# Kernel tuning notes

Hardware: AMD Instinct MI355X
Metric: run time of the kernel (lower is better)

Reference implementation:

```python
import jax, jax.numpy as jnp
import numpy as np

S, T, B = 50, 50, 64
SRC_V, TRG_V = 36616, 23262
E, EH, DH = 300, 512, 1024


def setup_inputs() -> dict:
    key = jax.random.key(0)
    ks = jax.random.split(key, 20)
    n = lambda k, shape: jax.random.normal(k, shape, jnp.float32) * 0.05
    return {
        "train_src_batch": jax.random.randint(ks[0], (S, B), 0, SRC_V),
        "train_trg_batch": jax.random.randint(ks[1], (T, B), 0, TRG_V),
        "emb_en": n(ks[2], (SRC_V, E)),
        "emb_de": n(ks[3], (TRG_V, E)),
        "enc_W_ih_f": n(ks[4], (4 * EH, E)),
        "enc_W_hh_f": n(ks[5], (4 * EH, EH)),
        "enc_b_f": n(ks[6], (4 * EH,)),
        "enc_W_ih_b": n(ks[7], (4 * EH, E)),
        "enc_W_hh_b": n(ks[8], (4 * EH, EH)),
        "enc_b_b": n(ks[9], (4 * EH,)),
        "dec_W_ih": n(ks[10], (4 * DH, E + DH)),
        "dec_W_hh": n(ks[11], (4 * DH, DH)),
        "dec_b": n(ks[12], (4 * DH,)),
        "W_gen": n(ks[13], (TRG_V, DH)),
        "b_gen": n(ks[14], (TRG_V,)),
        "W_i": n(ks[15], (DH, DH)),
        "W_o": n(ks[16], (DH, 2 * DH)),
    }


def _lstm_step(x, h, c, W_ih, W_hh, b):
    # PyTorch gate order: i, f, g, o
    gates = x @ W_ih.T + h @ W_hh.T + b
    i, f, g, o = jnp.split(gates, 4, axis=-1)
    c_new = jax.nn.sigmoid(f) * c + jax.nn.sigmoid(i) * jnp.tanh(g)
    h_new = jax.nn.sigmoid(o) * jnp.tanh(c_new)
    return h_new, c_new


def _run_lstm(x_seq, W_ih, W_hh, b, hidden):
    h0 = jnp.zeros((x_seq.shape[1], hidden), x_seq.dtype)
    def step(carry, x):
        h, c = carry
        h, c = _lstm_step(x, h, c, W_ih, W_hh, b)
        return (h, c), h
    (h, c), hs = jax.lax.scan(step, (h0, h0), x_seq)
    return hs, h, c


def _forward(train_src_batch, train_trg_batch, emb_en, emb_de,
             enc_W_ih_f, enc_W_hh_f, enc_b_f, enc_W_ih_b, enc_W_hh_b, enc_b_b,
             dec_W_ih, dec_W_hh, dec_b, W_gen, b_gen, W_i, W_o):
    x = emb_en[train_src_batch]                       # [S,B,E]
    hs_f, hf, cf = _run_lstm(x, enc_W_ih_f, enc_W_hh_f, enc_b_f, EH)
    hs_b, hb, cb = _run_lstm(x[::-1], enc_W_ih_b, enc_W_hh_b, enc_b_b, EH)
    output_hs = jnp.concatenate([hs_f, hs_b[::-1]], axis=-1)  # [S,B,1024]
    # Faithful to h.contiguous().view(B,1024) on direction-major [2,B,512]
    h = jnp.reshape(jnp.stack([hf, hb], axis=0), (B, DH))
    c = jnp.reshape(jnp.stack([cf, cb], axis=0), (B, DH))

    emb_trg = emb_de[train_trg_batch[: T - 1]]        # [T-1,B,E]

    def step(carry, e):
        h, c = carry
        # score[j,b] = output_hs[j,b] . (W_i h[b])  (the diag of the original mm)
        scores = jnp.einsum('sbd,bd->sb', output_hs, h @ W_i.T)
        # legacy nn.Softmax() on 2D input -> softmax over dim=1 (batch axis)
        a = jax.nn.softmax(scores, axis=1)
        s_t = jnp.einsum('sb,sbd->bd', a, output_hs)
        c_t = jnp.tanh(jnp.concatenate([s_t, h], axis=1) @ W_o.T)
        dec_in = jnp.concatenate([c_t, e], axis=1)    # [B, 1024+300]
        h, c = _lstm_step(dec_in, h, c, dec_W_ih, dec_W_hh, dec_b)
        logp = jax.nn.log_softmax(h @ W_gen.T + b_gen, axis=1)
        return (h, c), logp

    _, outs = jax.lax.scan(step, (h, c), emb_trg)     # [T-1,B,V]
    out0 = jnp.zeros((1, B, TRG_V), outs.dtype)       # output[0] filled with 0
    return jnp.concatenate([out0, outs], axis=0)      # [T,B,V]


def reference(train_src_batch, train_trg_batch, emb_en, emb_de,
              enc_W_ih_f, enc_W_hh_f, enc_b_f, enc_W_ih_b, enc_W_hh_b, enc_b_b,
              dec_W_ih, dec_W_hh, dec_b, W_gen, b_gen, W_i, W_o):
    return _forward(train_src_batch, train_trg_batch, emb_en, emb_de,
                    enc_W_ih_f, enc_W_hh_f, enc_b_f, enc_W_ih_b, enc_W_hh_b, enc_b_b,
                    dec_W_ih, dec_W_hh, dec_b, W_gen, b_gen, W_i, W_o)
```

## Files before the change

kernel.cpp:

```cpp
#include <hip/hip_runtime.h>
#include <hip/hip_bf16.h>

#define SS 50
#define TT 50
#define BB 64
#define TRGV 23262
#define EE 300
#define EH 512
#define DH 1024

#define GMRE 3136
#define GMP 3200
#define GK 1024
#define GNRE TRGV
#define GNP 23296

typedef short bf16x8 __attribute__((ext_vector_type(8)));
typedef float f32x4 __attribute__((ext_vector_type(4)));

__device__ __forceinline__ void glds16(const void* g, void* l) {
  __builtin_amdgcn_global_load_lds(
      (const __attribute__((address_space(1))) void*)g,
      (__attribute__((address_space(3))) void*)l, 16, 0, 0);
}

__device__ __forceinline__ float sigm(float x) { return 1.f / (1.f + expf(-x)); }
__device__ __forceinline__ float sum4(f32x4 v) { return v[0] + v[1] + v[2] + v[3]; }

__device__ __forceinline__ void split2(float x, __hip_bfloat16& hi, __hip_bfloat16& lo) {
  hi = __float2bfloat16(x);
  lo = __float2bfloat16(x - __bfloat162float(hi));
}

__device__ __forceinline__ void gbar(unsigned* arrive, unsigned* gen, int nblk) {
  __syncthreads();
  unsigned g = __hip_atomic_load(gen, __ATOMIC_RELAXED, __HIP_MEMORY_SCOPE_AGENT);
  if (threadIdx.x == 0)
    __hip_atomic_store(arrive + blockIdx.x, g + 1u, __ATOMIC_RELEASE, __HIP_MEMORY_SCOPE_AGENT);
  if (blockIdx.x == 0) {
    int i = threadIdx.x;
    if (i < nblk) {
      while (__hip_atomic_load(arrive + i, __ATOMIC_RELAXED, __HIP_MEMORY_SCOPE_AGENT) < g + 1u)
        __builtin_amdgcn_s_sleep(1);
      (void)__hip_atomic_load(arrive + i, __ATOMIC_ACQUIRE, __HIP_MEMORY_SCOPE_AGENT);
    }
    __syncthreads();
    if (threadIdx.x == 0)
      __hip_atomic_store(gen, g + 1u, __ATOMIC_RELEASE, __HIP_MEMORY_SCOPE_AGENT);
  }
  if (threadIdx.x == 0) {
    while (__hip_atomic_load(gen, __ATOMIC_RELAXED, __HIP_MEMORY_SCOPE_AGENT) < g + 1u)
      __builtin_amdgcn_s_sleep(1);
    (void)__hip_atomic_load(gen, __ATOMIC_ACQUIRE, __HIP_MEMORY_SCOPE_AGENT);
  }
  __syncthreads();
}

__global__ void k_zero(float* __restrict__ p, long n) {
  long i = (long)blockIdx.x * 256 + threadIdx.x;
  if (i < n) p[i] = 0.f;
}
__global__ void k_zero_bf(__hip_bfloat16* __restrict__ p, long n) {
  long i = (long)blockIdx.x * 256 + threadIdx.x;
  if (i < n) p[i] = __float2bfloat16(0.f);
}

__global__ void k_embed(const int* __restrict__ src, const float* __restrict__ emb,
                        float* __restrict__ x) {
  int id = blockIdx.x * 256 + threadIdx.x;
  if (id >= SS * BB * EE) return;
  int sb = id / EE, e = id % EE;
  x[id] = emb[(long)src[sb] * EE + e];
}

__global__ void k_dbperm(const float* __restrict__ db, float* __restrict__ dbp) {
  int id = blockIdx.x * 256 + threadIdx.x;
  if (id >= 4096) return;
  int u = id >> 2, g = id & 3;
  dbp[id] = db[g * 1024 + u];
}

__global__ void k_split_pad(const float* __restrict__ in, int ld_in, int col_off,
                            int Kreal, int Kpad, int rows_real, long rows_pad,
                            int mode, __hip_bfloat16* __restrict__ out) {
  long id = (long)blockIdx.x * 256 + threadIdx.x;
  if (id >= rows_pad * Kpad) return;
  long r = id / Kpad;
  int k = id % Kpad;
  float v = 0.f;
  if (r < rows_real && k < Kreal) {
    if (mode == 3) {
      v = in[(long)k * ld_in + col_off + r];
    } else {
      long sr = r;
      if (mode == 1) sr = ((49 - (r >> 6)) << 6) + (r & 63);
      else if (mode == 2) sr = (long)(r & 3) * 1024 + (r >> 2);
      v = in[sr * ld_in + col_off + k];
    }
  }
  __hip_bfloat16 hi, lo;
  split2(v, hi, lo);
  out[r * 2 * Kpad + k] = hi;
  out[r * 2 * Kpad + Kpad + k] = lo;
}

__global__ void k_embgather_split(const int* __restrict__ trg, const float* __restrict__ emb,
                                  __hip_bfloat16* __restrict__ out) {
  long id = (long)blockIdx.x * 256 + threadIdx.x;
  if (id >= 3200L * 320) return;
  long r = id / 320;
  int k = id % 320;
  int t = r >> 6, b = r & 63;
  float v = 0.f;
  if (t < TT - 1 && k < EE) v = emb[(long)trg[t * BB + b] * EE + k];
  __hip_bfloat16 hi, lo;
  split2(v, hi, lo);
  out[r * 640 + k] = hi;
  out[r * 640 + 320 + k] = lo;
}

__global__ void k_tobf16_pad(const float* __restrict__ W, __hip_bfloat16* __restrict__ Wb,
                             long nrow_real, long nrow_pad, int K) {
  long id = (long)blockIdx.x * 256 + threadIdx.x;
  if (id >= nrow_pad * K) return;
  long r = id / K;
  Wb[id] = __float2bfloat16(r < nrow_real ? W[id] : 0.f);
}

__global__ void k_repackT(const float* __restrict__ in, float* __restrict__ out) {
  long id = (long)blockIdx.x * 256 + threadIdx.x;
  if (id >= 3200L * 1024) return;
  long r = id >> 10;
  int n = id & 1023;
  out[((long)(n >> 2) * 3200 + r) * 4 + (n & 3)] = in[id];
}

template<int OUTBF>
__global__ __launch_bounds__(256) void k_gsplit(
    const __hip_bfloat16* __restrict__ A2, const __hip_bfloat16* __restrict__ W2,
    const float* __restrict__ bias, void* __restrict__ Cout,
    int Mreal, int Nreal, int ldc, int Kpad) {
  __shared__ __hip_bfloat16 As[128 * 32];
  __shared__ __hip_bfloat16 Bs[128 * 32];
  int tid = threadIdx.x, lane = tid & 63, w = tid >> 6;
  long m0 = (long)blockIdx.y * 128, n0 = (long)blockIdx.x * 128;
  int lda2 = 2 * Kpad;
  int srow = lane >> 2;
  int scol = (lane & 3) * 8;
  char* lA0 = (char*)As + w * 2048;
  char* lA1 = lA0 + 1024;
  char* lB0 = (char*)Bs + w * 2048;
  char* lB1 = lB0 + 1024;
  int wm = (w >> 1) * 64, wn = (w & 1) * 64;
  int fr = lane & 15;
  int kc = (lane >> 4) * 8;
  f32x4 acc[4][4] = {};

  for (int seg = 0; seg < 3; ++seg) {
    const __hip_bfloat16* Ab = A2 + (seg == 1 ? Kpad : 0);
    const __hip_bfloat16* Wb = W2 + (seg == 2 ? Kpad : 0);
    const __hip_bfloat16* gA0 = Ab + (m0 + w * 32 + srow) * (long)lda2 + scol;
    const __hip_bfloat16* gA1 = gA0 + 16L * lda2;
    const __hip_bfloat16* gB0 = Wb + (n0 + w * 32 + srow) * (long)lda2 + scol;
    const __hip_bfloat16* gB1 = gB0 + 16L * lda2;
    for (int kt = 0; kt < Kpad / 32; ++kt) {
      int k0 = kt * 32;
      glds16(gA0 + k0, lA0);
      glds16(gA1 + k0, lA1);
      glds16(gB0 + k0, lB0);
      glds16(gB1 + k0, lB1);
      __syncthreads();
      bf16x8 a[4], b[4];
      for (int mi = 0; mi < 4; ++mi)
        a[mi] = *(const bf16x8*)(As + (wm + mi * 16 + fr) * 32 + kc);
      for (int ni = 0; ni < 4; ++ni)
        b[ni] = *(const bf16x8*)(Bs + (wn + ni * 16 + fr) * 32 + kc);
      for (int mi = 0; mi < 4; ++mi)
        for (int ni = 0; ni < 4; ++ni)
          acc[mi][ni] = __builtin_amdgcn_mfma_f32_16x16x32_bf16(a[mi], b[ni], acc[mi][ni], 0, 0, 0);
      __syncthreads();
    }
  }

  for (int mi = 0; mi < 4; ++mi) {
    for (int ni = 0; ni < 4; ++ni) {
      int n = (int)n0 + wn + ni * 16 + (lane & 15);
      if (n >= Nreal) continue;
      float bv = bias ? bias[n] : 0.f;
      for (int r = 0; r < 4; ++r) {
        int m = (int)m0 + wm + mi * 16 + (lane >> 4) * 4 + r;
        if (m >= Mreal) continue;
        float v = acc[mi][ni][r] + bv;
        if (OUTBF) ((__hip_bfloat16*)Cout)[(long)m * ldc + n] = __float2bfloat16(v);
        else ((float*)Cout)[(long)m * ldc + n] = v;
      }
    }
  }
}

__global__ __launch_bounds__(512) void persist_enc(
    const float* __restrict__ xW_f, const float* __restrict__ xW_b,
    const float* __restrict__ Whf, const float* __restrict__ Whb,
    float* __restrict__ hs, float* hA, float* hB, float* hA2, float* hB2,
    float* __restrict__ cf, float* __restrict__ cb,
    float* __restrict__ hd0, float* __restrict__ hT0, float* __restrict__ cdD,
    unsigned* __restrict__ bar) {
  __shared__ float WL[16 * 516];
  int t = threadIdx.x;
  int blk = blockIdx.x;
  int dir = blk >> 7, bl = blk & 127;
  const float* Whh = dir ? Whb : Whf;
  const float* xWb0 = dir ? xW_b : xW_f;
  float* c = dir ? cb : cf;
  float* hp = dir ? hA2 : hA;
  float* hn = dir ? hB2 : hB;
  unsigned* arrive = bar;
  unsigned* gen = bar + 256;

  for (int idx = t; idx < 16 * 512; idx += 512) {
    int r = idx >> 9, k = idx & 511;
    int srcrow = (r & 3) * 512 + (bl * 4 + (r >> 2));
    WL[r * 516 + k] = Whh[(long)srcrow * 512 + k];
  }
  __syncthreads();

  int j = t & 15;
  int b0 = t >> 4, b1 = b0 + 32;
  int g = j & 3;
  int ju = bl * 4 + (j >> 2);
  int lbase = (t & 63) & ~3;
  const f32x4* wq = (const f32x4*)(WL + j * 516);

  for (int s = 0; s < SS; ++s) {
    const f32x4* h0q = (const f32x4*)(hp + b0 * 512);
    const f32x4* h1q = (const f32x4*)(hp + b1 * 512);
    f32x4 v0 = {0, 0, 0, 0}, v1 = {0, 0, 0, 0};
    for (int q = 0; q < 128; ++q) {
      f32x4 wv = wq[q];
      v0 += wv * h0q[q];
      v1 += wv * h1q[q];
    }
    const float* xW = xWb0 + (long)(s * BB) * 2048;
    float a0 = sum4(v0) + xW[b0 * 2048 + g * 512 + ju];
    float a1 = sum4(v1) + xW[b1 * 2048 + g * 512 + ju];
    float gi0 = __shfl(a0, lbase + 0), gf0 = __shfl(a0, lbase + 1);
    float gg0 = __shfl(a0, lbase + 2), go0 = __shfl(a0, lbase + 3);
    float gi1 = __shfl(a1, lbase + 0), gf1 = __shfl(a1, lbase + 1);
    float gg1 = __shfl(a1, lbase + 2), go1 = __shfl(a1, lbase + 3);
    if ((t & 3) == 0) {
      int hscol = dir ? (512 + ju) : ju;
      int srow = dir ? (SS - 1 - s) : s;
      long hsrow0 = (long)(srow * BB + b0) * DH + hscol;
      long hsrow1 = (long)(srow * BB + b1) * DH + hscol;
      float cn0 = sigm(gf0) * c[b0 * 512 + ju] + sigm(gi0) * tanhf(gg0);
      float hn0 = sigm(go0) * tanhf(cn0);
      c[b0 * 512 + ju] = cn0;
      hn[b0 * 512 + ju] = hn0;
      hs[hsrow0] = hn0;
      float cn1 = sigm(gf1) * c[b1 * 512 + ju] + sigm(gi1) * tanhf(gg1);
      float hn1 = sigm(go1) * tanhf(cn1);
      c[b1 * 512 + ju] = cn1;
      hn[b1 * 512 + ju] = hn1;
      hs[hsrow1] = hn1;
    }
    float* tmp = hp; hp = hn; hn = tmp;
    gbar(arrive, gen, 256);
  }
  int gid = blk * 512 + t;
  if (gid < 65536) {
    int d2 = gid >> 15, b = (gid >> 9) & 63, j2 = gid & 511;
    float hv = (d2 ? hA2 : hA)[b * 512 + j2];
    float cv = (d2 ? cb : cf)[b * 512 + j2];
    hd0[gid] = hv;
    cdD[gid] = cv;
    int bp = gid >> 10, jp = gid & 1023;
    hT0[jp * 64 + bp] = hv;
  }
}

__global__ __launch_bounds__(512) void persist_dec(
    const float* __restrict__ G, const float* __restrict__ HsWo1T,
    const float* __restrict__ Wo, const float* __restrict__ dWih,
    const float* __restrict__ dWhh, const __hip_bfloat16* __restrict__ Eg,
    float* hd0, float* hd1, float* hT0, float* hT1,
    float* __restrict__ cd, float* __restrict__ attw, float* __restrict__ ctb,
    __hip_bfloat16* __restrict__ A_bf, unsigned* __restrict__ bar) {
  __shared__ float WcL[16 * 2052];
  __shared__ float WoL[4 * 1028];
  __shared__ float red[2048];
  int t = threadIdx.x;
  int blk = blockIdx.x;
  int w = t >> 6, lane = t & 63;
  unsigned* arrive = bar;
  unsigned* gen = bar + 256;

  for (int idx = t; idx < 16 * 2048; idx += 512) {
    int r = idx >> 11, k = idx & 2047;
    int rp2 = blk * 16 + r;
    long srcrow = (long)(rp2 & 3) * 1024 + (rp2 >> 2);
    float v = (k < 1024) ? dWih[srcrow * 1324 + k] : dWhh[srcrow * 1024 + (k - 1024)];
    WcL[r * 2052 + k] = v;
  }
  for (int idx = t; idx < 4 * 1024; idx += 512) {
    int r = idx >> 10, k = idx & 1023;
    WoL[r * 1028 + k] = Wo[(long)(blk * 4 + r) * 2048 + 1024 + k];
  }
  __syncthreads();

  float* hcur = hd0; float* hnew = hd1;
  float* hTc = hT0;  float* hTn = hT1;
  int j = t & 15;
  int b0 = t >> 4, b1 = b0 + 32;
  int rp = blk * 16 + j;
  int ju = blk * 4 + (j >> 2);
  int lbase = (t & 63) & ~3;
  const f32x4* hw = (const f32x4*)(HsWo1T + (long)blk * 3200 * 4);

  for (int ts = 0; ts < TT - 1; ++ts) {
    if (blk < SS) {
      int s = blk;
      const f32x4* gq = (const f32x4*)(G + ((long)(s * BB + lane)) * DH + w * 128);
      const f32x4* hq = (const f32x4*)(hcur + lane * DH + w * 128);
      f32x4 a4 = {0, 0, 0, 0};
      for (int q = 0; q < 32; ++q) a4 += gq[q] * hq[q];
      red[w * 64 + lane] = sum4(a4);
      __syncthreads();
      if (w == 0) {
        float sc = 0.f;
        for (int i = 0; i < 8; ++i) sc += red[i * 64 + lane];
        float m = sc;
        for (int o = 32; o > 0; o >>= 1) m = fmaxf(m, __shfl_xor(m, o));
        float e = expf(sc - m);
        float su = e;
        for (int o = 32; o > 0; o >>= 1) su += __shfl_xor(su, o);
        attw[s * BB + lane] = e / su;
      }
    }
    gbar(arrive, gen, 256);
    {
      int n0 = blk * 4;
      f32x4 z = {0, 0, 0, 0};
      for (int s = w; s < SS; s += 8) {
        float aw = attw[s * BB + lane];
        f32x4 hv = hw[s * 64 + lane];
        z += aw * hv;
      }
      for (int k = w * 128; k < w * 128 + 128; ++k) {
        float hb = hTc[k * 64 + lane];
        f32x4 wv = {WoL[0 * 1028 + k], WoL[1 * 1028 + k], WoL[2 * 1028 + k], WoL[3 * 1028 + k]};
        z += hb * wv;
      }
      red[w * 256 + lane * 4 + 0] = z[0];
      red[w * 256 + lane * 4 + 1] = z[1];
      red[w * 256 + lane * 4 + 2] = z[2];
      red[w * 256 + lane * 4 + 3] = z[3];
      __syncthreads();
      if (t < 256) {
        int b = t >> 2, nl = t & 3;
        float sv = 0.f;
        for (int i = 0; i < 8; ++i) sv += red[i * 256 + b * 4 + nl];
        ctb[b * DH + n0 + nl] = tanhf(sv);
      }
    }
    gbar(arrive, gen, 256);
    {
      const f32x4* wq1 = (const f32x4*)(WcL + j * 2052);
      const f32x4* wq2 = (const f32x4*)(WcL + j * 2052 + 1024);
      const f32x4* c0q = (const f32x4*)(ctb + b0 * DH);
      const f32x4* c1q = (const f32x4*)(ctb + b1 * DH);
      const f32x4* h0q = (const f32x4*)(hcur + b0 * DH);
      const f32x4* h1q = (const f32x4*)(hcur + b1 * DH);
      f32x4 v0 = {0, 0, 0, 0}, v1 = {0, 0, 0, 0};
      for (int q = 0; q < 256; ++q) {
        f32x4 wv = wq1[q];
        v0 += wv * c0q[q];
        v1 += wv * c1q[q];
      }
      for (int q = 0; q < 256; ++q) {
        f32x4 wv = wq2[q];
        v0 += wv * h0q[q];
        v1 += wv * h1q[q];
      }
      float a0 = sum4(v0) + __bfloat162float(Eg[((long)(ts * BB + b0)) * 4096 + rp]);
      float a1 = sum4(v1) + __bfloat162float(Eg[((long)(ts * BB + b1)) * 4096 + rp]);
      float gi0 = __shfl(a0, lbase + 0), gf0 = __shfl(a0, lbase + 1);
      float gg0 = __shfl(a0, lbase + 2), go0 = __shfl(a0, lbase + 3);
      float gi1 = __shfl(a1, lbase + 0), gf1 = __shfl(a1, lbase + 1);
      float gg1 = __shfl(a1, lbase + 2), go1 = __shfl(a1, lbase + 3);
      if ((t & 3) == 0) {
        float cn0 = sigm(gf0) * cd[b0 * DH + ju] + sigm(gi0) * tanhf(gg0);
        float hn0 = sigm(go0) * tanhf(cn0);
        cd[b0 * DH + ju] = cn0;
        hnew[b0 * DH + ju] = hn0;
        hTn[ju * 64 + b0] = hn0;
        A_bf[(long)ts * (BB * DH) + b0 * DH + ju] = __float2bfloat16(hn0);
        float cn1 = sigm(gf1) * cd[b1 * DH + ju] + sigm(gi1) * tanhf(gg1);
        float hn1 = sigm(go1) * tanhf(cn1);
        cd[b1 * DH + ju] = cn1;
        hnew[b1 * DH + ju] = hn1;
        hTn[ju * 64 + b1] = hn1;
        A_bf[(long)ts * (BB * DH) + b1 * DH + ju] = __float2bfloat16(hn1);
      }
    }
    { float* x = hcur; hcur = hnew; hnew = x; }
    { float* x = hTc; hTc = hTn; hTn = x; }
    gbar(arrive, gen, 256);
  }
}

__global__ __launch_bounds__(256) void k_gen_mfma(
    const __hip_bfloat16* __restrict__ A, const __hip_bfloat16* __restrict__ Bw,
    const float* __restrict__ bias, float* __restrict__ C) {
  __shared__ __hip_bfloat16 As[128 * 32];
  __shared__ __hip_bfloat16 Bs[128 * 32];
  int tid = threadIdx.x;
  int lane = tid & 63, w = tid >> 6;
  long m0 = (long)blockIdx.y * 128, n0 = (long)blockIdx.x * 128;
  int srow = lane >> 2;
  int scol = (lane & 3) * 8;
  const __hip_bfloat16* gA0 = A + (m0 + w * 32 + srow) * GK + scol;
  const __hip_bfloat16* gA1 = gA0 + 16 * GK;
  const __hip_bfloat16* gB0 = Bw + (n0 + w * 32 + srow) * GK + scol;
  const __hip_bfloat16* gB1 = gB0 + 16 * GK;
  char* lA0 = (char*)As + w * 2048;
  char* lA1 = lA0 + 1024;
  char* lB0 = (char*)Bs + w * 2048;
  char* lB1 = lB0 + 1024;
  int wm = (w >> 1) * 64, wn = (w & 1) * 64;
  int fr = lane & 15;
  int kc = (lane >> 4) * 8;
  f32x4 acc[4][4] = {};
  for (int kt = 0; kt < GK / 32; ++kt) {
    int k0 = kt * 32;
    glds16(gA0 + k0, lA0);
    glds16(gA1 + k0, lA1);
    glds16(gB0 + k0, lB0);
    glds16(gB1 + k0, lB1);
    __syncthreads();
    bf16x8 a[4], b[4];
    for (int mi = 0; mi < 4; ++mi)
      a[mi] = *(const bf16x8*)(As + (wm + mi * 16 + fr) * 32 + kc);
    for (int ni = 0; ni < 4; ++ni)
      b[ni] = *(const bf16x8*)(Bs + (wn + ni * 16 + fr) * 32 + kc);
    for (int mi = 0; mi < 4; ++mi)
      for (int ni = 0; ni < 4; ++ni)
        acc[mi][ni] = __builtin_amdgcn_mfma_f32_16x16x32_bf16(a[mi], b[ni], acc[mi][ni], 0, 0, 0);
    __syncthreads();
  }
  for (int mi = 0; mi < 4; ++mi) {
    for (int ni = 0; ni < 4; ++ni) {
      int n = (int)n0 + wn + ni * 16 + (lane & 15);
      if (n >= GNRE) continue;
      float bv = bias[n];
      for (int r = 0; r < 4; ++r) {
        int m = (int)m0 + wm + mi * 16 + (lane >> 4) * 4 + r;
        if (m < GMRE) C[(long)m * TRGV + n] = acc[mi][ni][r] + bv;
      }
    }
  }
}

__global__ __launch_bounds__(256) void k_logsoftmax(float* __restrict__ out) {
  int r = blockIdx.x;
  float* p = out + (long)(BB + r) * TRGV;
  int tid = threadIdx.x;
  __shared__ float red[256];
  float m = -1e30f;
  for (int i = tid; i < TRGV; i += 256) m = fmaxf(m, p[i]);
  red[tid] = m;
  __syncthreads();
  for (int s = 128; s > 0; s >>= 1) {
    if (tid < s) red[tid] = fmaxf(red[tid], red[tid + s]);
    __syncthreads();
  }
  m = red[0];
  __syncthreads();
  float sum = 0.f;
  for (int i = tid; i < TRGV; i += 256) sum += expf(p[i] - m);
  red[tid] = sum;
  __syncthreads();
  for (int s = 128; s > 0; s >>= 1) {
    if (tid < s) red[tid] += red[tid + s];
    __syncthreads();
  }
  float lse = m + logf(red[0]);
  for (int i = tid; i < TRGV; i += 256) p[i] -= lse;
}

extern "C" void kernel_launch(void* const* d_in, const int* in_sizes, int n_in,
                              void* d_out, int out_size, void* d_ws, size_t ws_size,
                              hipStream_t stream) {
  const int* src = (const int*)d_in[0];
  const int* trg = (const int*)d_in[1];
  const float* emb_en = (const float*)d_in[2];
  const float* emb_de = (const float*)d_in[3];
  const float* eWih_f = (const float*)d_in[4];
  const float* eWhh_f = (const float*)d_in[5];
  const float* eb_f = (const float*)d_in[6];
  const float* eWih_b = (const float*)d_in[7];
  const float* eWhh_b = (const float*)d_in[8];
  const float* eb_b = (const float*)d_in[9];
  const float* dWih = (const float*)d_in[10];
  const float* dWhh = (const float*)d_in[11];
  const float* db = (const float*)d_in[12];
  const float* Wgen = (const float*)d_in[13];
  const float* bgen = (const float*)d_in[14];
  const float* Wi = (const float*)d_in[15];
  const float* Wo = (const float*)d_in[16];
  float* out = (float*)d_out;

  float* base = (float*)d_ws;
  __hip_bfloat16* xsf = (__hip_bfloat16*)base;
  __hip_bfloat16* xsb = (__hip_bfloat16*)(base + 1024000);
  __hip_bfloat16* Wihf2 = (__hip_bfloat16*)(base + 2048000);
  __hip_bfloat16* Wihb2 = (__hip_bfloat16*)(base + 2703360);
  float* xW_f = base + 3358720;
  float* xW_b = base + 9912320;
  __hip_bfloat16* hs2 = (__hip_bfloat16*)base;
  __hip_bfloat16* Wi2 = (__hip_bfloat16*)(base + 3276800);
  __hip_bfloat16* Wo12 = (__hip_bfloat16*)(base + 4325376);
  __hip_bfloat16* eg2 = (__hip_bfloat16*)(base + 5373952);
  __hip_bfloat16* Wce2 = (__hip_bfloat16*)(base + 6397952);
  __hip_bfloat16* E_g = (__hip_bfloat16*)(base + 7708672);
  __hip_bfloat16* Wgen_bf = (__hip_bfloat16*)base;
  float* p = base + 16465920;
  float* x_enc = p; p += SS * BB * EE;
  float* hs = p; p += (long)SS * BB * DH;
  float* G = p; p += (long)SS * BB * DH;
  float* HsWo1 = p; p += (long)SS * BB * DH;
  float* HsWo1T = p; p += (long)SS * BB * DH;
  __hip_bfloat16* A_bf = (__hip_bfloat16*)p; p += (GMP * GK) / 2;
  float* dbp = p; p += 4096;
  float* attw = p; p += SS * BB;
  float* hd0 = p; p += BB * DH;
  float* hd1 = p; p += BB * DH;
  float* hT0 = p; p += BB * DH;
  float* hT1 = p; p += BB * DH;
  float* cd = p; p += BB * DH;
  float* ctb = p; p += BB * DH;
  float* hA = p; p += BB * EH;
  float* hB = p; p += BB * EH;
  float* hA2 = p; p += BB * EH;
  float* hB2 = p; p += BB * EH;
  float* cf = p; p += BB * EH;
  float* cb = p; p += BB * EH;
  unsigned* bar = (unsigned*)p; p += 512;

  dim3 b256(256);

  k_embed<<<dim3((SS * BB * EE + 255) / 256), b256, 0, stream>>>(src, emb_en, x_enc);
  k_zero<<<dim3((6 * BB * EH + 255) / 256), b256, 0, stream>>>(hA, 6 * BB * EH);
  k_zero<<<dim3(2), b256, 0, stream>>>((float*)bar, 512);
  k_zero<<<dim3((int)(((long)BB * TRGV + 255) / 256)), b256, 0, stream>>>(out, (long)BB * TRGV);
  k_zero_bf<<<dim3(((GMP - GMRE) * GK + 255) / 256), b256, 0, stream>>>(
      A_bf + (long)GMRE * GK, (long)(GMP - GMRE) * GK);
  k_dbperm<<<dim3(16), b256, 0, stream>>>(db, dbp);

  k_split_pad<<<dim3((3200 * 320 + 255) / 256), b256, 0, stream>>>(
      x_enc, EE, 0, EE, 320, 3200, 3200, 0, xsf);
  k_split_pad<<<dim3((3200 * 320 + 255) / 256), b256, 0, stream>>>(
      x_enc, EE, 0, EE, 320, 3200, 3200, 1, xsb);
  k_split_pad<<<dim3((2048 * 320 + 255) / 256), b256, 0, stream>>>(
      eWih_f, EE, 0, EE, 320, 2048, 2048, 0, Wihf2);
  k_split_pad<<<dim3((2048 * 320 + 255) / 256), b256, 0, stream>>>(
      eWih_b, EE, 0, EE, 320, 2048, 2048, 0, Wihb2);
  k_gsplit<0><<<dim3(16, 25), b256, 0, stream>>>(xsf, Wihf2, eb_f, xW_f, 3200, 2048, 2048, 320);
  k_gsplit<0><<<dim3(16, 25), b256, 0, stream>>>(xsb, Wihb2, eb_b, xW_b, 3200, 2048, 2048, 320);

  {
    void* args[] = {(void*)&xW_f, (void*)&xW_b, (void*)&eWhh_f, (void*)&eWhh_b,
                    (void*)&hs, (void*)&hA, (void*)&hB, (void*)&hA2, (void*)&hB2,
                    (void*)&cf, (void*)&cb, (void*)&hd0, (void*)&hT0, (void*)&cd,
                    (void*)&bar};
    hipLaunchCooperativeKernel((const void*)persist_enc, dim3(256), dim3(512),
                               args, 0, stream);
  }

  k_split_pad<<<dim3((int)((3200L * 1024 + 255) / 256)), b256, 0, stream>>>(
      hs, DH, 0, DH, 1024, 3200, 3200, 0, hs2);
  k_split_pad<<<dim3((int)((1024L * 1024 + 255) / 256)), b256, 0, stream>>>(
      Wi, DH, 0, DH, 1024, 1024, 1024, 3, Wi2);
  k_split_pad<<<dim3((int)((1024L * 1024 + 255) / 256)), b256, 0, stream>>>(
      Wo, 2 * DH, 0, DH, 1024, 1024, 1024, 0, Wo12);
  k_embgather_split<<<dim3((int)((3200L * 320 + 255) / 256)), b256, 0, stream>>>(
      trg, emb_de, eg2);
  k_split_pad<<<dim3((int)((4096L * 320 + 255) / 256)), b256, 0, stream>>>(
      dWih, 1324, 1024, EE, 320, 4096, 4096, 2, Wce2);
  k_gsplit<0><<<dim3(8, 25), b256, 0, stream>>>(hs2, Wi2, (const float*)nullptr, G, 3200, 1024, 1024, 1024);
  k_gsplit<0><<<dim3(8, 25), b256, 0, stream>>>(hs2, Wo12, (const float*)nullptr, HsWo1, 3200, 1024, 1024, 1024);
  k_repackT<<<dim3((int)((3200L * 1024 + 255) / 256)), b256, 0, stream>>>(HsWo1, HsWo1T);
  k_gsplit<1><<<dim3(32, 25), b256, 0, stream>>>(eg2, Wce2, dbp, E_g, 3136, 4096, 4096, 320);

  {
    void* args[] = {(void*)&G, (void*)&HsWo1T, (void*)&Wo, (void*)&dWih, (void*)&dWhh,
                    (void*)&E_g, (void*)&hd0, (void*)&hd1, (void*)&hT0, (void*)&hT1,
                    (void*)&cd, (void*)&attw, (void*)&ctb, (void*)&A_bf, (void*)&bar};
    hipLaunchCooperativeKernel((const void*)persist_dec, dim3(256), dim3(512),
                               args, 0, stream);
  }

  k_tobf16_pad<<<dim3((int)(((long)GNP * GK + 255) / 256)), b256, 0, stream>>>(
      Wgen, Wgen_bf, GNRE, GNP, GK);
  k_gen_mfma<<<dim3(GNP / 128, GMP / 128), b256, 0, stream>>>(
      A_bf, Wgen_bf, bgen, out + (long)BB * TRGV);
  k_logsoftmax<<<dim3((TT - 1) * BB), b256, 0, stream>>>(out);
}
```

Before: 7.570 ms.

## Split encoder barrier per direction, widen decoder blocks and overlap context matvec

The encoder's grid barrier is split so each direction's 128 blocks synchronise only among themselves, with one full barrier at the end. The decoder goes to 1024 threads per block, so each thread handles one batch row instead of two. The h·Wo2 part of the context product is moved before the attention barrier so it overlaps with score computation. Wo is stored in LDS as interleaved bf16, and the embedding gate term is prefetched early. These trade lower barrier cost and more parallelism for extra register and LDS pressure and bf16 rounding of Wo.

```diff
diff --git a/kernel.cpp b/kernel.cpp
--- a/kernel.cpp
+++ b/kernel.cpp
@@ -26,20 +26,25 @@
 
 __device__ __forceinline__ float sigm(float x) { return 1.f / (1.f + expf(-x)); }
 __device__ __forceinline__ float sum4(f32x4 v) { return v[0] + v[1] + v[2] + v[3]; }
+__device__ __forceinline__ float bfu2f(unsigned short u) {
+  unsigned int x = ((unsigned)u) << 16;
+  return __uint_as_float(x);
+}
 
 __device__ __forceinline__ void split2(float x, __hip_bfloat16& hi, __hip_bfloat16& lo) {
   hi = __float2bfloat16(x);
   lo = __float2bfloat16(x - __bfloat162float(hi));
 }
 
-__device__ __forceinline__ void gbar(unsigned* arrive, unsigned* gen, int nblk) {
+__device__ __forceinline__ void gbarg(unsigned* arrive, unsigned* gen,
+                                      int idxInGrp, int n, bool poller) {
   __syncthreads();
   unsigned g = __hip_atomic_load(gen, __ATOMIC_RELAXED, __HIP_MEMORY_SCOPE_AGENT);
   if (threadIdx.x == 0)
-    __hip_atomic_store(arrive + blockIdx.x, g + 1u, __ATOMIC_RELEASE, __HIP_MEMORY_SCOPE_AGENT);
-  if (blockIdx.x == 0) {
+    __hip_atomic_store(arrive + idxInGrp, g + 1u, __ATOMIC_RELEASE, __HIP_MEMORY_SCOPE_AGENT);
+  if (poller) {
     int i = threadIdx.x;
-    if (i < nblk) {
+    if (i < n) {
       while (__hip_atomic_load(arrive + i, __ATOMIC_RELAXED, __HIP_MEMORY_SCOPE_AGENT) < g + 1u)
         __builtin_amdgcn_s_sleep(1);
       (void)__hip_atomic_load(arrive + i, __ATOMIC_ACQUIRE, __HIP_MEMORY_SCOPE_AGENT);
@@ -214,8 +219,10 @@
   float* c = dir ? cb : cf;
   float* hp = dir ? hA2 : hA;
   float* hn = dir ? hB2 : hB;
-  unsigned* arrive = bar;
-  unsigned* gen = bar + 256;
+  unsigned* arrG = bar + dir * 128;
+  unsigned* genG = bar + 784 + dir * 16;
+  unsigned* arrA = bar + 256;
+  unsigned* genA = bar + 816;
 
   for (int idx = t; idx < 16 * 512; idx += 512) {
     int r = idx >> 9, k = idx & 511;
@@ -264,8 +271,9 @@
       hs[hsrow1] = hn1;
     }
     float* tmp = hp; hp = hn; hn = tmp;
-    gbar(arrive, gen, 256);
-  }
+    gbarg(arrG, genG, bl, 128, bl == 0);
+  }
+  gbarg(arrA, genA, blk, 256, blk == 0);
   int gid = blk * 512 + t;
   if (gid < 65536) {
     int d2 = gid >> 15, b = (gid >> 9) & 63, j2 = gid & 511;
@@ -278,7 +286,7 @@
   }
 }
 
-__global__ __launch_bounds__(512) void persist_dec(
+__global__ __launch_bounds__(1024) void persist_dec(
     const float* __restrict__ G, const float* __restrict__ HsWo1T,
     const float* __restrict__ Wo, const float* __restrict__ dWih,
     const float* __restrict__ dWhh, const __hip_bfloat16* __restrict__ Eg,
@@ -286,125 +294,110 @@
     float* __restrict__ cd, float* __restrict__ attw, float* __restrict__ ctb,
     __hip_bfloat16* __restrict__ A_bf, unsigned* __restrict__ bar) {
   __shared__ float WcL[16 * 2052];
-  __shared__ float WoL[4 * 1028];
-  __shared__ float red[2048];
+  __shared__ __hip_bfloat16 WoLi[1024 * 4];
+  __shared__ float red[4096];
   int t = threadIdx.x;
   int blk = blockIdx.x;
   int w = t >> 6, lane = t & 63;
-  unsigned* arrive = bar;
-  unsigned* gen = bar + 256;
-
-  for (int idx = t; idx < 16 * 2048; idx += 512) {
+  int j = t & 15, b = t >> 4;
+  unsigned* arrive = bar + 512;
+  unsigned* gen = bar + 832;
+
+  for (int idx = t; idx < 16 * 2048; idx += 1024) {
     int r = idx >> 11, k = idx & 2047;
     int rp2 = blk * 16 + r;
     long srcrow = (long)(rp2 & 3) * 1024 + (rp2 >> 2);
     float v = (k < 1024) ? dWih[srcrow * 1324 + k] : dWhh[srcrow * 1024 + (k - 1024)];
     WcL[r * 2052 + k] = v;
   }
-  for (int idx = t; idx < 4 * 1024; idx += 512) {
+  for (int idx = t; idx < 4 * 1024; idx += 1024) {
     int r = idx >> 10, k = idx & 1023;
-    WoL[r * 1028 + k] = Wo[(long)(blk * 4 + r) * 2048 + 1024 + k];
+    WoLi[k * 4 + r] = __float2bfloat16(Wo[(long)(blk * 4 + r) * 2048 + 1024 + k]);
   }
   __syncthreads();
 
   float* hcur = hd0; float* hnew = hd1;
   float* hTc = hT0;  float* hTn = hT1;
-  int j = t & 15;
-  int b0 = t >> 4, b1 = b0 + 32;
   int rp = blk * 16 + j;
   int ju = blk * 4 + (j >> 2);
   int lbase = (t & 63) & ~3;
-  const f32x4* hw = (const f32x4*)(HsWo1T + (long)blk * 3200 * 4);
+  const f32x4* hw4 = (const f32x4*)(HsWo1T + (long)blk * 3200 * 4);
+  f32x4* red4 = (f32x4*)red;
 
   for (int ts = 0; ts < TT - 1; ++ts) {
+    float eg = bfu2f(((const unsigned short*)Eg)[((long)(ts * BB + b)) * 4096 + rp]);
+    f32x4 z1 = {0, 0, 0, 0};
+    for (int k = w * 64; k < w * 64 + 64; ++k) {
+      float hb = hTc[k * 64 + lane];
+      const unsigned short* wv4 = (const unsigned short*)(WoLi + k * 4);
+      f32x4 wv = {bfu2f(wv4[0]), bfu2f(wv4[1]), bfu2f(wv4[2]), bfu2f(wv4[3])};
+      z1 += hb * wv;
+    }
     if (blk < SS) {
       int s = blk;
-      const f32x4* gq = (const f32x4*)(G + ((long)(s * BB + lane)) * DH + w * 128);
-      const f32x4* hq = (const f32x4*)(hcur + lane * DH + w * 128);
+      const f32x4* gq = (const f32x4*)(G + ((long)(s * BB + lane)) * DH + w * 64);
+      const f32x4* hq = (const f32x4*)(hcur + lane * DH + w * 64);
       f32x4 a4 = {0, 0, 0, 0};
-      for (int q = 0; q < 32; ++q) a4 += gq[q] * hq[q];
+      for (int q = 0; q < 16; ++q) a4 += gq[q] * hq[q];
       red[w * 64 + lane] = sum4(a4);
       __syncthreads();
-      if (w == 0) {
+      if (t < 64) {
         float sc = 0.f;
-        for (int i = 0; i < 8; ++i) sc += red[i * 64 + lane];
+        for (int i = 0; i < 16; ++i) sc += red[i * 64 + t];
         float m = sc;
         for (int o = 32; o > 0; o >>= 1) m = fmaxf(m, __shfl_xor(m, o));
         float e = expf(sc - m);
         float su = e;
         for (int o = 32; o > 0; o >>= 1) su += __shfl_xor(su, o);
-        attw[s * BB + lane] = e / su;
+        attw[s * BB + t] = e / su;
       }
-    }
-    gbar(arrive, gen, 256);
+      __syncthreads();
+    }
+    red4[w * 64 + lane] = z1;
+    gbarg(arrive, gen, blk, 256, blk == 0);
+
     {
-      int n0 = blk * 4;
-      f32x4 z = {0, 0, 0, 0};
-      for (int s = w; s < SS; s += 8) {
+      f32x4 z2 = {0, 0, 0, 0};
+      for (int s = w; s < SS; s += 16) {
         float aw = attw[s * BB + lane];
-        f32x4 hv = hw[s * 64 + lane];
-        z += aw * hv;
+        z2 += aw * hw4[s * 64 + lane];
       }
-      for (int k = w * 128; k < w * 128 + 128; ++k) {
-        float hb = hTc[k * 64 + lane];
-        f32x4 wv = {WoL[0 * 1028 + k], WoL[1 * 1028 + k], WoL[2 * 1028 + k], WoL[3 * 1028 + k]};
-        z += hb * wv;
-      }
-      red[w * 256 + lane * 4 + 0] = z[0];
-      red[w * 256 + lane * 4 + 1] = z[1];
-      red[w * 256 + lane * 4 + 2] = z[2];
-      red[w * 256 + lane * 4 + 3] = z[3];
+      red4[w * 64 + lane] += z2;
       __syncthreads();
       if (t < 256) {
-        int b = t >> 2, nl = t & 3;
+        int bb = t >> 2, nl = t & 3;
         float sv = 0.f;
-        for (int i = 0; i < 8; ++i) sv += red[i * 256 + b * 4 + nl];
-        ctb[b * DH + n0 + nl] = tanhf(sv);
+        for (int i = 0; i < 16; ++i) sv += red[(i * 64 + bb) * 4 + nl];
+        ctb[bb * DH + blk * 4 + nl] = tanhf(sv);
       }
     }
-    gbar(arrive, gen, 256);
+    gbarg(arrive, gen, blk, 256, blk == 0);
+
     {
       const f32x4* wq1 = (const f32x4*)(WcL + j * 2052);
       const f32x4* wq2 = (const f32x4*)(WcL + j * 2052 + 1024);
-      const f32x4* c0q = (const f32x4*)(ctb + b0 * DH);
-      const f32x4* c1q = (const f32x4*)(ctb + b1 * DH);
-      const f32x4* h0q = (const f32x4*)(hcur + b0 * DH);
-      const f32x4* h1q = (const f32x4*)(hcur + b1 * DH);
-      f32x4 v0 = {0, 0, 0, 0}, v1 = {0, 0, 0, 0};
-      for (int q = 0; q < 256; ++q) {
-        f32x4 wv = wq1[q];
-        v0 += wv * c0q[q];
-        v1 += wv * c1q[q];
-      }
-      for (int q = 0; q < 256; ++q) {
-        f32x4 wv = wq2[q];
-        v0 += wv * h0q[q];
-        v1 += wv * h1q[q];
-      }
-      float a0 = sum4(v0) + __bfloat162float(Eg[((long)(ts * BB + b0)) * 4096 + rp]);
-      float a1 = sum4(v1) + __bfloat162float(Eg[((long)(ts * BB + b1)) * 4096 + rp]);
+      const f32x4* c0q = (const f32x4*)(ctb + b * DH);
+      const f32x4* h0q = (const f32x4*)(hcur + b * DH);
+      f32x4 v0 = {0, 0, 0, 0};
+      #pragma unroll 8
+      for (int q = 0; q < 256; ++q) v0 += wq1[q] * c0q[q];
+      #pragma unroll 8
+      for (int q = 0; q < 256; ++q) v0 += wq2[q] * h0q[q];
+      float a0 = sum4(v0) + eg;
       float gi0 = __shfl(a0, lbase + 0), gf0 = __shfl(a0, lbase + 1);
       float gg0 = __shfl(a0, lbase + 2), go0 = __shfl(a0, lbase + 3);
-      float gi1 = __shfl(a1, lbase + 0), gf1 = __shfl(a1, lbase + 1);
-      float gg1 = __shfl(a1, lbase + 2), go1 = __shfl(a1, lbase + 3);
       if ((t & 3) == 0) {
-        float cn0 = sigm(gf0) * cd[b0 * DH + ju] + sigm(gi0) * tanhf(gg0);
+        float cn0 = sigm(gf0) * cd[b * DH + ju] + sigm(gi0) * tanhf(gg0);
         float hn0 = sigm(go0) * tanhf(cn0);
-        cd[b0 * DH + ju] = cn0;
-        hnew[b0 * DH + ju] = hn0;
-        hTn[ju * 64 + b0] = hn0;
-        A_bf[(long)ts * (BB * DH) + b0 * DH + ju] = __float2bfloat16(hn0);
-        float cn1 = sigm(gf1) * cd[b1 * DH + ju] + sigm(gi1) * tanhf(gg1);
-        float hn1 = sigm(go1) * tanhf(cn1);
-        cd[b1 * DH + ju] = cn1;
-        hnew[b1 * DH + ju] = hn1;
-        hTn[ju * 64 + b1] = hn1;
-        A_bf[(long)ts * (BB * DH) + b1 * DH + ju] = __float2bfloat16(hn1);
+        cd[b * DH + ju] = cn0;
+        hnew[b * DH + ju] = hn0;
+        hTn[ju * 64 + b] = hn0;
+        A_bf[(long)ts * (BB * DH) + b * DH + ju] = __float2bfloat16(hn0);
       }
     }
     { float* x = hcur; hcur = hnew; hnew = x; }
     { float* x = hTc; hTc = hTn; hTn = x; }
-    gbar(arrive, gen, 256);
+    gbarg(arrive, gen, blk, 256, blk == 0);
   }
 }
 
@@ -544,13 +537,13 @@
   float* hB2 = p; p += BB * EH;
   float* cf = p; p += BB * EH;
   float* cb = p; p += BB * EH;
-  unsigned* bar = (unsigned*)p; p += 512;
+  unsigned* bar = (unsigned*)p; p += 1024;
 
   dim3 b256(256);
 
   k_embed<<<dim3((SS * BB * EE + 255) / 256), b256, 0, stream>>>(src, emb_en, x_enc);
   k_zero<<<dim3((6 * BB * EH + 255) / 256), b256, 0, stream>>>(hA, 6 * BB * EH);
-  k_zero<<<dim3(2), b256, 0, stream>>>((float*)bar, 512);
+  k_zero<<<dim3(4), b256, 0, stream>>>((float*)bar, 1024);
   k_zero<<<dim3((int)(((long)BB * TRGV + 255) / 256)), b256, 0, stream>>>(out, (long)BB * TRGV);
   k_zero_bf<<<dim3(((GMP - GMRE) * GK + 255) / 256), b256, 0, stream>>>(
       A_bf + (long)GMRE * GK, (long)(GMP - GMRE) * GK);
@@ -595,7 +588,7 @@
     void* args[] = {(void*)&G, (void*)&HsWo1T, (void*)&Wo, (void*)&dWih, (void*)&dWhh,
                     (void*)&E_g, (void*)&hd0, (void*)&hd1, (void*)&hT0, (void*)&hT1,
                     (void*)&cd, (void*)&attw, (void*)&ctb, (void*)&A_bf, (void*)&bar};
-    hipLaunchCooperativeKernel((const void*)persist_dec, dim3(256), dim3(512),
+    hipLaunchCooperativeKernel((const void*)persist_dec, dim3(256), dim3(1024),
                                args, 0, stream);
   }
 
```

After: 7.882 ms. +4.1%, slower.
